# Performance work log

Measured on AMD Instinct MI355X. Metric: run time of the kernel, lower is better.

The kernel has to match this reference:

```python
import jax, jax.numpy as jnp
import numpy as np

N, E, B = 30000, 480000, 64
F_IN, HID, ED = 128, 64, 32
NEG, EPS = 0.2, 1e-5


def _add_self_loops(edge_index, edge_attr):
    # PyG add_self_loops with fill_value='mean': self-loop edge_attr of node i
    # is the mean of edge_attr over edges whose destination is i.
    src, dst = edge_index[0], edge_index[1]
    cnt = jax.ops.segment_sum(jnp.ones((edge_attr.shape[0],), edge_attr.dtype), dst, num_segments=N)
    mean = jax.ops.segment_sum(edge_attr, dst, num_segments=N) / jnp.maximum(cnt, 1.0)[:, None]
    loop = jnp.arange(N)
    return jnp.concatenate([src, loop]), jnp.concatenate([dst, loop]), jnp.concatenate([edge_attr, mean], axis=0)


def _gat_conv(x, src, dst, ea, W, We, a_s, a_d, a_e, bias, H, Fo):
    xs = (x @ W).reshape(-1, H, Fo)              # [N, H, Fo]
    al_src = (xs * a_s).sum(-1)                  # [N, H]
    al_dst = (xs * a_d).sum(-1)                  # [N, H]
    ef = (ea @ We).reshape(-1, H, Fo)            # [Et, H, Fo]
    alpha = al_src[src] + al_dst[dst] + (ef * a_e).sum(-1)   # [Et, H]
    alpha = jax.nn.leaky_relu(alpha, NEG)
    # softmax over incoming edges of each destination node (segment softmax)
    m = jax.ops.segment_max(alpha, dst, num_segments=N)
    ex = jnp.exp(alpha - m[dst])
    s = jax.ops.segment_sum(ex, dst, num_segments=N)
    w = ex / s[dst]                              # [Et, H]
    out = jax.ops.segment_sum(xs[src] * w[:, :, None], dst, num_segments=N)
    return out.reshape(-1, H * Fo) + bias


def _bn(x, g, b):
    # BatchNorm1d in training mode: biased batch statistics over nodes
    mu = x.mean(0)
    var = x.var(0)
    return (x - mu) * jax.lax.rsqrt(var + EPS) * g + b


def _pool(x, batch, Wg, bg):
    # GlobalAttention: softmax(gate_nn(x)) per graph, weighted sum of x
    gate = (x @ Wg + bg)[:, 0]                   # [N]
    m = jax.ops.segment_max(gate, batch, num_segments=B)
    e = jnp.exp(gate - m[batch])
    s = jax.ops.segment_sum(e, batch, num_segments=B)
    w = e / s[batch]
    return jax.ops.segment_sum(x * w[:, None], batch, num_segments=B)   # [B, HID]


def setup_inputs():
    k = jax.random.split(jax.random.key(0), 16)
    g = lambda i, shape, fan: jax.random.normal(k[i], shape, jnp.float32) / np.sqrt(fan)
    return {
        "x": jax.random.normal(k[0], (N, F_IN), jnp.float32),
        "edge_attr": jax.random.normal(k[1], (E, ED), jnp.float32),
        "edge_index": jax.random.randint(k[2], (2, E), 0, N),
        "batch": jnp.sort(jax.random.randint(k[3], (N,), 0, B)),
        "W1": g(4, (F_IN, 4 * HID), F_IN),
        "We1": g(5, (ED, 4 * HID), ED),
        "att_src1": g(6, (4, HID), HID),
        "att_dst1": g(7, (4, HID), HID),
        "att_edge1": g(8, (4, HID), HID),
        "bias1": jnp.zeros((4 * HID,), jnp.float32),
        "g1": jnp.ones((4 * HID,), jnp.float32),
        "b1": jnp.zeros((4 * HID,), jnp.float32),
        "W2": g(9, (4 * HID, HID), 4 * HID),
        "We2": g(10, (ED, HID), ED),
        "att_src2": g(11, (1, HID), HID),
        "att_dst2": g(12, (1, HID), HID),
        "att_edge2": g(13, (1, HID), HID),
        "bias2": jnp.zeros((HID,), jnp.float32),
        "g2": jnp.ones((HID,), jnp.float32),
        "b2": jnp.zeros((HID,), jnp.float32),
        "Wg": g(14, (HID, 1), HID),
        "bg": jnp.zeros((1,), jnp.float32),
    }


def reference(x, edge_attr, edge_index, batch, W1, We1, att_src1, att_dst1, att_edge1, bias1, g1, b1, W2, We2, att_src2, att_dst2, att_edge2, bias2, g2, b2, Wg, bg):
    src, dst, ea = _add_self_loops(edge_index, edge_attr)
    h = jax.nn.relu(_bn(_gat_conv(x, src, dst, ea, W1, We1, att_src1, att_dst1, att_edge1, bias1, 4, HID), g1, b1))
    h = jax.nn.relu(_bn(_gat_conv(h, src, dst, ea, W2, We2, att_src2, att_dst2, att_edge2, bias2, 1, HID), g2, b2))
    return _pool(h, batch, Wg, bg)
```

## Files before the change

kernel.cpp:

```cpp
#include <hip/hip_runtime.h>
#include <math.h>

#define NN 30000
#define EE 480000
#define BB 64

typedef __bf16 b16x8 __attribute__((ext_vector_type(8)));
typedef float  f32x4 __attribute__((ext_vector_type(4)));
typedef unsigned short u16x8 __attribute__((ext_vector_type(8)));

__device__ __forceinline__ float wsum64(float v){
  #pragma unroll
  for (int m = 32; m >= 1; m >>= 1) v += __shfl_xor(v, m, 64);
  return v;
}
__device__ __forceinline__ float wmax64(float v){
  #pragma unroll
  for (int m = 32; m >= 1; m >>= 1) v = fmaxf(v, __shfl_xor(v, m, 64));
  return v;
}
__device__ __forceinline__ float wsum16(float v){
  #pragma unroll
  for (int m = 1; m < 16; m <<= 1) v += __shfl_xor(v, m, 64);
  return v;
}
__device__ __forceinline__ unsigned short f2b(float f){
  union { float f; unsigned u; } v; v.f = f;
  unsigned r = v.u + 0x7fffu + ((v.u >> 16) & 1u);
  return (unsigned short)(r >> 16);
}
__device__ __forceinline__ float b2f(unsigned short u){
  union { unsigned u; float f; } v; v.u = ((unsigned)u) << 16;
  return v.f;
}

__global__ void hist_kernel(const int* __restrict__ dst, int* __restrict__ deg){
  int e = blockIdx.x*256 + threadIdx.x;
  if (e < EE) atomicAdd(&deg[dst[e]], 1);
}

__global__ __launch_bounds__(1024) void scan_kernel(const int* __restrict__ deg, int* __restrict__ rowptr){
  __shared__ int s[1024];
  int tid = threadIdx.x;
  const int PER = 30;
  int base = tid * PER;
  int sum = 0;
  for (int j = 0; j < PER; j++){ int idx = base+j; if (idx < NN) sum += deg[idx]; }
  s[tid] = sum; __syncthreads();
  for (int off = 1; off < 1024; off <<= 1){
    int v = 0;
    if (tid >= off) v = s[tid-off];
    __syncthreads();
    s[tid] += v;
    __syncthreads();
  }
  int run = s[tid] - sum;
  for (int j = 0; j < PER; j++){
    int idx = base+j;
    if (idx < NN){ rowptr[idx] = run; run += deg[idx]; }
  }
  if (tid == 1023) rowptr[NN] = s[1023];
}

__global__ void prep_kernel(const float* __restrict__ W1, const float* __restrict__ W2,
                            const float* __restrict__ We1, const float* __restrict__ ae1,
                            const float* __restrict__ We2, const float* __restrict__ ae2,
                            unsigned short* __restrict__ W1t, unsigned short* __restrict__ W2t,
                            float* __restrict__ wae){
  int t = threadIdx.x;
  if (blockIdx.x == 0){
    for (int k = 0; k < 128; k++) W1t[t*128 + k] = f2b(W1[k*256 + t]);
    if (t < 64){
      for (int k = 0; k < 256; k++) W2t[t*256 + k] = f2b(W2[k*64 + t]);
    }
  } else {
    if (t < 128){
      int h = t >> 5, k = t & 31;
      float s = 0.f;
      for (int f = 0; f < 64; f++) s += We1[k*256 + h*64 + f] * ae1[h*64 + f];
      wae[h*32 + k] = s;
    } else if (t < 160){
      int k = t - 128;
      float s = 0.f;
      for (int f = 0; f < 64; f++) s += We2[k*64 + f] * ae2[f];
      wae[128 + k] = s;
    }
  }
}

__global__ __launch_bounds__(256) void edot_scatter_kernel(const float* __restrict__ ea,
    const float* __restrict__ wae, const int* __restrict__ src, const int* __restrict__ dst,
    const int* __restrict__ rowptr, int* __restrict__ cursor,
    int* __restrict__ srccsr, float* __restrict__ edot1, float* __restrict__ edot2){
  __shared__ float s_w[160];
  if (threadIdx.x < 160) s_w[threadIdx.x] = wae[threadIdx.x];
  __syncthreads();
  const int il = threadIdx.x & 7;
  const int e = blockIdx.x*32 + (threadIdx.x >> 3);
  if (e >= EE) return;
  float4 v = *(const float4*)(ea + (size_t)e*32 + il*4);
  float dots[5];
  #pragma unroll
  for (int h = 0; h < 5; h++){
    float4 w = *(const float4*)&s_w[h*32 + il*4];
    dots[h] = v.x*w.x + v.y*w.y + v.z*w.z + v.w*w.w;
  }
  #pragma unroll
  for (int m = 1; m < 8; m <<= 1)
    #pragma unroll
    for (int h = 0; h < 5; h++) dots[h] += __shfl_xor(dots[h], m, 64);
  if (il == 0){
    int dd = dst[e];
    int slot = rowptr[dd] + atomicAdd(&cursor[dd], 1);
    srccsr[slot] = src[e];
    float4 o; o.x = dots[0]; o.y = dots[1]; o.z = dots[2]; o.w = dots[3];
    *(float4*)(edot1 + (size_t)slot*4) = o;
    edot2[slot] = dots[4];
  }
}

__global__ __launch_bounds__(256) void gemm1_mfma(const float* __restrict__ x,
    const unsigned short* __restrict__ Bt, const float* __restrict__ a_s, const float* __restrict__ a_d,
    unsigned short* __restrict__ out, float* __restrict__ alsrc, float* __restrict__ aldst){
  __shared__ unsigned short As[128*136];
  __shared__ unsigned short Bs[64*136];
  const int tid = threadIdx.x;
  const int w = tid >> 6, lane = tid & 63;
  const int c = lane & 15, gq = lane >> 4;
  const int m0 = blockIdx.x * 128;
  #pragma unroll
  for (int q = 0; q < 16; q++){
    int ch = tid*16 + q;
    int r = ch >> 5, off = (ch & 31)*4;
    int grow = m0 + r;
    ushort4 o;
    if (grow < NN){
      float4 v = *(const float4*)(x + (size_t)grow*128 + off);
      o.x = f2b(v.x); o.y = f2b(v.y); o.z = f2b(v.z); o.w = f2b(v.w);
    } else o = make_ushort4(0,0,0,0);
    *(ushort4*)&As[r*136 + off] = o;
  }
  #pragma unroll
  for (int q = 0; q < 4; q++){
    int ch = tid*4 + q;
    int n = ch >> 4, off = (ch & 15)*8;
    *(ulonglong2*)&Bs[n*136 + off] = *(const ulonglong2*)(Bt + (size_t)n*128 + off);
  }
  __syncthreads();
  for (int head = 0; head < 4; head++){
    f32x4 acc[2][4];
    #pragma unroll
    for (int mt = 0; mt < 2; mt++)
      #pragma unroll
      for (int nt = 0; nt < 4; nt++) acc[mt][nt] = (f32x4){0.f,0.f,0.f,0.f};
    #pragma unroll
    for (int k0 = 0; k0 < 128; k0 += 32){
      b16x8 afr[2], bfr[4];
      #pragma unroll
      for (int mt = 0; mt < 2; mt++)
        afr[mt] = *(const b16x8*)&As[(w*32 + mt*16 + c)*136 + k0 + gq*8];
      #pragma unroll
      for (int nt = 0; nt < 4; nt++)
        bfr[nt] = *(const b16x8*)&Bs[(nt*16 + c)*136 + k0 + gq*8];
      #pragma unroll
      for (int mt = 0; mt < 2; mt++)
        #pragma unroll
        for (int nt = 0; nt < 4; nt++)
          acc[mt][nt] = __builtin_amdgcn_mfma_f32_16x16x32_bf16(afr[mt], bfr[nt], acc[mt][nt], 0, 0, 0);
    }
    __syncthreads();
    if (head < 3){
      #pragma unroll
      for (int q = 0; q < 4; q++){
        int ch = tid*4 + q;
        int n = ch >> 4, off = (ch & 15)*8;
        *(ulonglong2*)&Bs[n*136 + off] = *(const ulonglong2*)(Bt + (size_t)((head+1)*64 + n)*128 + off);
      }
    }
    float asv[4], adv[4];
    #pragma unroll
    for (int nt = 0; nt < 4; nt++){
      asv[nt] = a_s[head*64 + nt*16 + c];
      adv[nt] = a_d[head*64 + nt*16 + c];
    }
    #pragma unroll
    for (int mt = 0; mt < 2; mt++){
      int base_row = m0 + w*32 + mt*16 + gq*4;
      #pragma unroll
      for (int r = 0; r < 4; r++){
        int row = base_row + r;
        float ps = 0.f, pd = 0.f;
        #pragma unroll
        for (int nt = 0; nt < 4; nt++){
          ps += acc[mt][nt][r] * asv[nt];
          pd += acc[mt][nt][r] * adv[nt];
        }
        ps = wsum16(ps); pd = wsum16(pd);
        if (row < NN){
          if (c == 0){
            alsrc[(size_t)row*4 + head] = ps;
            aldst[(size_t)row*4 + head] = pd;
          }
          #pragma unroll
          for (int nt = 0; nt < 4; nt++)
            out[(size_t)row*256 + head*64 + nt*16 + c] = f2b(acc[mt][nt][r]);
        }
      }
    }
    if (head < 3) __syncthreads();
  }
}

__global__ __launch_bounds__(256) void gemm2_mfma(const unsigned short* __restrict__ Ab,
    const unsigned short* __restrict__ Bt,
    const float* __restrict__ cs, const float* __restrict__ csq,
    const float* __restrict__ g, const float* __restrict__ b,
    const float* __restrict__ a_s, const float* __restrict__ a_d,
    unsigned short* __restrict__ out, float* __restrict__ alsrc, float* __restrict__ aldst){
  __shared__ unsigned short As[128*136];
  __shared__ unsigned short Bs[64*136];
  __shared__ float s_scale[256], s_shift[256];
  const int tid = threadIdx.x;
  const int w = tid >> 6, lane = tid & 63;
  const int c = lane & 15, gq = lane >> 4;
  const int m0 = blockIdx.x * 128;
  if (tid < 256){
    float mu  = cs[tid]  * (1.f/NN);
    float var = csq[tid] * (1.f/NN) - mu*mu;
    float rs  = rsqrtf(var + 1e-5f);
    float sc  = rs * g[tid];
    s_scale[tid] = sc;
    s_shift[tid] = b[tid] - mu*sc;
  }
  __syncthreads();
  f32x4 acc[2][4];
  #pragma unroll
  for (int mt = 0; mt < 2; mt++)
    #pragma unroll
    for (int nt = 0; nt < 4; nt++) acc[mt][nt] = (f32x4){0.f,0.f,0.f,0.f};
  for (int kp = 0; kp < 256; kp += 128){
    #pragma unroll
    for (int q = 0; q < 16; q++){
      int ch = tid*16 + q;
      int r = ch >> 5, off = (ch & 31)*4;
      int grow = m0 + r;
      ushort4 o;
      if (grow < NN){
        ushort4 v = *(const ushort4*)(Ab + (size_t)grow*256 + kp + off);
        float4 sc = *(const float4*)&s_scale[kp + off];
        float4 sh = *(const float4*)&s_shift[kp + off];
        o.x = f2b(fmaxf(fmaf(b2f(v.x), sc.x, sh.x), 0.f));
        o.y = f2b(fmaxf(fmaf(b2f(v.y), sc.y, sh.y), 0.f));
        o.z = f2b(fmaxf(fmaf(b2f(v.z), sc.z, sh.z), 0.f));
        o.w = f2b(fmaxf(fmaf(b2f(v.w), sc.w, sh.w), 0.f));
      } else o = make_ushort4(0,0,0,0);
      *(ushort4*)&As[r*136 + off] = o;
    }
    #pragma unroll
    for (int q = 0; q < 4; q++){
      int ch = tid*4 + q;
      int n = ch >> 4, off = (ch & 15)*8;
      *(ulonglong2*)&Bs[n*136 + off] = *(const ulonglong2*)(Bt + (size_t)n*256 + kp + off);
    }
    __syncthreads();
    #pragma unroll
    for (int k0 = 0; k0 < 128; k0 += 32){
      b16x8 afr[2], bfr[4];
      #pragma unroll
      for (int mt = 0; mt < 2; mt++)
        afr[mt] = *(const b16x8*)&As[(w*32 + mt*16 + c)*136 + k0 + gq*8];
      #pragma unroll
      for (int nt = 0; nt < 4; nt++)
        bfr[nt] = *(const b16x8*)&Bs[(nt*16 + c)*136 + k0 + gq*8];
      #pragma unroll
      for (int mt = 0; mt < 2; mt++)
        #pragma unroll
        for (int nt = 0; nt < 4; nt++)
          acc[mt][nt] = __builtin_amdgcn_mfma_f32_16x16x32_bf16(afr[mt], bfr[nt], acc[mt][nt], 0, 0, 0);
    }
    __syncthreads();
  }
  float asv[4], adv[4];
  #pragma unroll
  for (int nt = 0; nt < 4; nt++){
    asv[nt] = a_s[nt*16 + c];
    adv[nt] = a_d[nt*16 + c];
  }
  #pragma unroll
  for (int mt = 0; mt < 2; mt++){
    int base_row = m0 + w*32 + mt*16 + gq*4;
    #pragma unroll
    for (int r = 0; r < 4; r++){
      int row = base_row + r;
      float ps = 0.f, pd = 0.f;
      #pragma unroll
      for (int nt = 0; nt < 4; nt++){
        ps += acc[mt][nt][r] * asv[nt];
        pd += acc[mt][nt][r] * adv[nt];
      }
      ps = wsum16(ps); pd = wsum16(pd);
      if (row < NN){
        if (c == 0){
          alsrc[row] = ps;
          aldst[row] = pd;
        }
        #pragma unroll
        for (int nt = 0; nt < 4; nt++)
          out[(size_t)row*64 + nt*16 + c] = f2b(acc[mt][nt][r]);
      }
    }
  }
}

template<int H>
__global__ __launch_bounds__(256) void agg_kernel(const int* __restrict__ rowptr,
    const int* __restrict__ src_csr, const float* __restrict__ edot,
    const float* __restrict__ al_src, const float* __restrict__ al_dst,
    const unsigned short* __restrict__ xsb, const float* __restrict__ bias,
    unsigned short* __restrict__ outb, float* __restrict__ outf){
  constexpr int CH = 128;
  __shared__ float s_e_all[4][CH*H];
  __shared__ int   s_src_all[4][CH];
  const int wid  = threadIdx.x >> 6;
  const int lane = threadIdx.x & 63;
  const int i = blockIdx.x*4 + wid;
  float* s_e  = s_e_all[wid];
  int*   s_src = s_src_all[wid];
  const int r0 = rowptr[i];
  const int d  = rowptr[i+1] - r0;
  float ad[H], asi[H];
  #pragma unroll
  for (int h = 0; h < H; h++){ ad[h] = al_dst[(size_t)i*H+h]; asi[h] = al_src[(size_t)i*H+h]; }
  float sesum[H], m[H];
  #pragma unroll
  for (int h = 0; h < H; h++){ sesum[h] = 0.f; m[h] = -1e30f; }
  for (int t = lane; t < d; t += 64){
    int s = r0 + t;
    int sn = src_csr[s];
    if (t < CH) s_src[t] = sn;
    float al[H];
    if constexpr (H == 4){
      float4 av = *(const float4*)(al_src + (size_t)sn*4);
      float4 ev = *(const float4*)(edot + (size_t)s*4);
      al[0]=av.x+ad[0]+ev.x; al[1]=av.y+ad[1]+ev.y; al[2]=av.z+ad[2]+ev.z; al[3]=av.w+ad[3]+ev.w;
      sesum[0]+=ev.x; sesum[1]+=ev.y; sesum[2]+=ev.z; sesum[3]+=ev.w;
    } else {
      float ev = edot[s];
      al[0] = al_src[sn] + ad[0] + ev;
      sesum[0] += ev;
    }
    #pragma unroll
    for (int h = 0; h < H; h++){
      float a = al[h]; a = a > 0.f ? a : 0.2f*a;
      if (t < CH) s_e[t*H+h] = a;
      m[h] = fmaxf(m[h], a);
    }
  }
  float invd = (d > 0) ? 1.f/(float)d : 0.f;
  float sa[H];
  #pragma unroll
  for (int h = 0; h < H; h++){
    sesum[h] = wsum64(sesum[h]);
    m[h] = wmax64(m[h]);
    float a = asi[h] + ad[h] + sesum[h]*invd;
    sa[h] = a > 0.f ? a : 0.2f*a;
    m[h] = fmaxf(m[h], sa[h]);
  }
  float acc8[8];
  #pragma unroll
  for (int j = 0; j < 8; j++) acc8[j] = 0.f;
  float dpart[H];
  #pragma unroll
  for (int h = 0; h < H; h++) dpart[h] = 0.f;
  const int half = lane >> 5, il5 = lane & 31;
  const int grp  = lane >> 3, il3 = lane & 7;
  int c0 = 0;
  while (c0 < d){
    int cl = min(CH, d - c0);
    if (c0 > 0){
      for (int t = lane; t < cl; t += 64){
        int s = r0 + c0 + t;
        int sn = src_csr[s];
        s_src[t] = sn;
        if constexpr (H == 4){
          float4 av = *(const float4*)(al_src + (size_t)sn*4);
          float4 ev = *(const float4*)(edot + (size_t)s*4);
          float a0=av.x+ad[0]+ev.x, a1=av.y+ad[1]+ev.y, a2=av.z+ad[2]+ev.z, a3=av.w+ad[3]+ev.w;
          s_e[t*4+0]=a0>0.f?a0:0.2f*a0; s_e[t*4+1]=a1>0.f?a1:0.2f*a1;
          s_e[t*4+2]=a2>0.f?a2:0.2f*a2; s_e[t*4+3]=a3>0.f?a3:0.2f*a3;
        } else {
          float a = al_src[sn] + ad[0] + edot[s];
          s_e[t] = a > 0.f ? a : 0.2f*a;
        }
      }
    }
    for (int t = lane; t < cl; t += 64){
      #pragma unroll
      for (int h = 0; h < H; h++){
        float e = __expf(s_e[t*H+h] - m[h]);
        s_e[t*H+h] = e;
        dpart[h] += e;
      }
    }
    __builtin_amdgcn_wave_barrier();
    if constexpr (H == 4){
      const int hd = il5 >> 3;
      for (int t = half; t < cl; t += 2){
        int sn = s_src[t];
        float wv = s_e[t*4 + hd];
        u16x8 u = *(const u16x8*)(xsb + (size_t)sn*256 + il5*8);
        #pragma unroll
        for (int j = 0; j < 8; j++) acc8[j] += wv * b2f(u[j]);
      }
    } else {
      for (int t = grp; t < cl; t += 8){
        int sn = s_src[t];
        float wv = s_e[t];
        u16x8 u = *(const u16x8*)(xsb + (size_t)sn*64 + il3*8);
        #pragma unroll
        for (int j = 0; j < 8; j++) acc8[j] += wv * b2f(u[j]);
      }
    }
    __builtin_amdgcn_wave_barrier();
    c0 += CH;
  }
  float es[H];
  #pragma unroll
  for (int h = 0; h < H; h++) es[h] = __expf(sa[h] - m[h]);
  if (lane == 0){
    #pragma unroll
    for (int h = 0; h < H; h++) dpart[h] += es[h];
  }
  if constexpr (H == 4){
    if (half == 0){
      float wv = es[il5 >> 3];
      u16x8 u = *(const u16x8*)(xsb + (size_t)i*256 + il5*8);
      #pragma unroll
      for (int j = 0; j < 8; j++) acc8[j] += wv * b2f(u[j]);
    }
  } else {
    if (grp == 0){
      float wv = es[0];
      u16x8 u = *(const u16x8*)(xsb + (size_t)i*64 + il3*8);
      #pragma unroll
      for (int j = 0; j < 8; j++) acc8[j] += wv * b2f(u[j]);
    }
  }
  float denom[H];
  #pragma unroll
  for (int h = 0; h < H; h++) denom[h] = wsum64(dpart[h]);
  if constexpr (H == 4){
    #pragma unroll
    for (int j = 0; j < 8; j++) acc8[j] += __shfl_xor(acc8[j], 32, 64);
    if (lane < 32){
      float inv = 1.f / denom[il5 >> 3];
      u16x8 o;
      #pragma unroll
      for (int j = 0; j < 8; j++) o[j] = f2b(acc8[j]*inv + bias[il5*8 + j]);
      *(u16x8*)(outb + (size_t)i*256 + il5*8) = o;
    }
  } else {
    #pragma unroll
    for (int j = 0; j < 8; j++){
      acc8[j] += __shfl_xor(acc8[j], 8, 64);
      acc8[j] += __shfl_xor(acc8[j], 16, 64);
      acc8[j] += __shfl_xor(acc8[j], 32, 64);
    }
    if (lane < 8){
      float inv = 1.f / denom[0];
      float4 o0, o1;
      o0.x = acc8[0]*inv + bias[il3*8+0]; o0.y = acc8[1]*inv + bias[il3*8+1];
      o0.z = acc8[2]*inv + bias[il3*8+2]; o0.w = acc8[3]*inv + bias[il3*8+3];
      o1.x = acc8[4]*inv + bias[il3*8+4]; o1.y = acc8[5]*inv + bias[il3*8+5];
      o1.z = acc8[6]*inv + bias[il3*8+6]; o1.w = acc8[7]*inv + bias[il3*8+7];
      *(float4*)(outf + (size_t)i*64 + il3*8)     = o0;
      *(float4*)(outf + (size_t)i*64 + il3*8 + 4) = o1;
    }
  }
}

__global__ __launch_bounds__(256) void bn_stats_b16_kernel(const unsigned short* __restrict__ h,
    float* __restrict__ cs, float* __restrict__ csq){
  __shared__ float s_red[4][256], q_red[4][256];
  const int tid = threadIdx.x;
  const int wv = tid >> 6, lane = tid & 63;
  const int rg = lane >> 5, cg = lane & 31;
  float s8[8], q8[8];
  #pragma unroll
  for (int j = 0; j < 8; j++){ s8[j] = 0.f; q8[j] = 0.f; }
  for (int chunk = blockIdx.x; chunk < 3750; chunk += 256){
    int r = chunk*8 + wv*2 + rg;
    u16x8 u = *(const u16x8*)(h + (size_t)r*256 + cg*8);
    #pragma unroll
    for (int j = 0; j < 8; j++){
      float v = b2f(u[j]);
      s8[j] += v; q8[j] += v*v;
    }
  }
  #pragma unroll
  for (int j = 0; j < 8; j++){
    s8[j] += __shfl_xor(s8[j], 32, 64);
    q8[j] += __shfl_xor(q8[j], 32, 64);
  }
  if (lane < 32){
    #pragma unroll
    for (int j = 0; j < 8; j++){
      s_red[wv][cg*8 + j] = s8[j];
      q_red[wv][cg*8 + j] = q8[j];
    }
  }
  __syncthreads();
  if (tid < 256){
    float ts = s_red[0][tid] + s_red[1][tid] + s_red[2][tid] + s_red[3][tid];
    float tq = q_red[0][tid] + q_red[1][tid] + q_red[2][tid] + q_red[3][tid];
    atomicAdd(&cs[tid], ts);
    atomicAdd(&csq[tid], tq);
  }
}

__global__ __launch_bounds__(256) void bn_stats_f32_kernel(const float* __restrict__ h,
    float* __restrict__ cs, float* __restrict__ csq){
  int col = threadIdx.x & 63;
  int ro  = threadIdx.x >> 6;
  float s = 0.f, s2 = 0.f;
  for (int r = blockIdx.x*4 + ro; r < NN; r += 1024){
    float v = h[(size_t)r*64 + col];
    s += v; s2 += v*v;
  }
  atomicAdd(&cs[col], s);
  atomicAdd(&csq[col], s2);
}

__global__ __launch_bounds__(256) void gate_kernel(const float* __restrict__ h,
    const float* __restrict__ cs, const float* __restrict__ csq,
    const float* __restrict__ g2, const float* __restrict__ b2,
    const float* __restrict__ Wg, const float* __restrict__ bg,
    float* __restrict__ hn, float* __restrict__ gate){
  int wid = threadIdx.x >> 6, lane = threadIdx.x & 63;
  int n = blockIdx.x*4 + wid;
  float mu  = cs[lane]  * (1.f/NN);
  float var = csq[lane] * (1.f/NN) - mu*mu;
  float rs  = rsqrtf(var + 1e-5f);
  float sc  = rs * g2[lane];
  float sh  = b2[lane] - mu*sc;
  float v = h[(size_t)n*64 + lane];
  float xx = fmaxf(fmaf(v, sc, sh), 0.f);
  hn[(size_t)n*64 + lane] = xx;
  float p = wsum64(xx * Wg[lane]);
  if (lane == 0) gate[n] = p + bg[0];
}

__global__ __launch_bounds__(256) void pool_kernel(const int* __restrict__ batch,
    const float* __restrict__ gate, const float* __restrict__ hn, float* __restrict__ out){
  __shared__ float red[256];
  __shared__ float a_red[4][64], w_red[4];
  __shared__ int seb[2];
  int b = blockIdx.x, tid = threadIdx.x;
  int wv = tid >> 6, lane = tid & 63;
  if (tid < 2){
    int target = b + tid;
    int lo = 0, hi = NN;
    while (lo < hi){ int mid = (lo+hi) >> 1; if (batch[mid] < target) lo = mid+1; else hi = mid; }
    seb[tid] = lo;
  }
  __syncthreads();
  int s = seb[0], e = seb[1];
  if (e <= s){ if (tid < 64) out[b*64 + tid] = 0.f; return; }
  float mloc = -1e30f;
  for (int n = s + tid; n < e; n += 256) mloc = fmaxf(mloc, gate[n]);
  mloc = wmax64(mloc);
  if (lane == 0) red[wv] = mloc;
  __syncthreads();
  float m = fmaxf(fmaxf(red[0], red[1]), fmaxf(red[2], red[3]));
  int rgrp = tid >> 4, cq = tid & 15;
  f32x4 acc = (f32x4){0.f,0.f,0.f,0.f};
  float wp = 0.f;
  for (int n = s + rgrp; n < e; n += 16){
    float wgt = __expf(gate[n] - m);
    float4 v = *(const float4*)(hn + (size_t)n*64 + cq*4);
    acc[0] += wgt*v.x; acc[1] += wgt*v.y; acc[2] += wgt*v.z; acc[3] += wgt*v.w;
    if (cq == 0) wp += wgt;
  }
  #pragma unroll
  for (int j = 0; j < 4; j++){
    acc[j] += __shfl_xor(acc[j], 16, 64);
    acc[j] += __shfl_xor(acc[j], 32, 64);
  }
  wp += __shfl_xor(wp, 16, 64);
  wp += __shfl_xor(wp, 32, 64);
  if (lane < 16){
    #pragma unroll
    for (int j = 0; j < 4; j++) a_red[wv][lane*4 + j] = acc[j];
  }
  if (lane == 0) w_red[wv] = wp;
  __syncthreads();
  if (tid < 64){
    float tot = a_red[0][tid] + a_red[1][tid] + a_red[2][tid] + a_red[3][tid];
    float wsm = w_red[0] + w_red[1] + w_red[2] + w_red[3];
    out[b*64 + tid] = tot / wsm;
  }
}

extern "C" void kernel_launch(void* const* d_in, const int* in_sizes, int n_in,
                              void* d_out, int out_size, void* d_ws, size_t ws_size,
                              hipStream_t stream){
  const float* x     = (const float*)d_in[0];
  const float* ea    = (const float*)d_in[1];
  const int*   ei    = (const int*)d_in[2];
  const int*   batch = (const int*)d_in[3];
  const float* W1    = (const float*)d_in[4];
  const float* We1   = (const float*)d_in[5];
  const float* as1   = (const float*)d_in[6];
  const float* ad1   = (const float*)d_in[7];
  const float* ae1   = (const float*)d_in[8];
  const float* bias1 = (const float*)d_in[9];
  const float* g1    = (const float*)d_in[10];
  const float* b1    = (const float*)d_in[11];
  const float* W2    = (const float*)d_in[12];
  const float* We2   = (const float*)d_in[13];
  const float* as2   = (const float*)d_in[14];
  const float* ad2   = (const float*)d_in[15];
  const float* ae2   = (const float*)d_in[16];
  const float* bias2 = (const float*)d_in[17];
  const float* g2    = (const float*)d_in[18];
  const float* b2    = (const float*)d_in[19];
  const float* Wg    = (const float*)d_in[20];
  const float* bg    = (const float*)d_in[21];
  const int* srcI = ei;
  const int* dstI = ei + EE;

  char* ws = (char*)d_ws;
  int*   deg    = (int*)(ws + 0);
  int*   cursor = (int*)(ws + 120064);
  float* stats  = (float*)(ws + 240128);
  int*   rowptr = (int*)(ws + 244224);
  int*   srccsr = (int*)(ws + 364288);
  float* wae    = (float*)(ws + 2284288);
  unsigned short* W1t = (unsigned short*)(ws + 2285056);
  unsigned short* W2t = (unsigned short*)(ws + 2350592);
  float* alsrc  = (float*)(ws + 2383360);
  float* aldst  = (float*)(ws + 2863360);
  float* gateb  = (float*)(ws + 3343360);
  float* edot1  = (float*)(ws + 3463424);
  float* edot2  = (float*)(ws + 11143424);
  unsigned short* xs1b = (unsigned short*)(ws + 13063424);
  unsigned short* h1b  = (unsigned short*)(ws + 28423424);
  unsigned short* xs2b = (unsigned short*)(ws + 43783424);
  float* h2     = (float*)(ws + 47623424);
  float* hn     = (float*)(ws + 55303424);

  (void)hipMemsetAsync(ws, 0, 244224, stream);

  hist_kernel<<<1875, 256, 0, stream>>>(dstI, deg);
  scan_kernel<<<1, 1024, 0, stream>>>(deg, rowptr);
  prep_kernel<<<2, 256, 0, stream>>>(W1, W2, We1, ae1, We2, ae2, W1t, W2t, wae);
  edot_scatter_kernel<<<15000, 256, 0, stream>>>(ea, wae, srcI, dstI, rowptr, cursor,
                                                 srccsr, edot1, edot2);

  gemm1_mfma<<<235, 256, 0, stream>>>(x, W1t, as1, ad1, xs1b, alsrc, aldst);
  agg_kernel<4><<<7500, 256, 0, stream>>>(rowptr, srccsr, edot1, alsrc, aldst, xs1b, bias1, h1b, nullptr);
  bn_stats_b16_kernel<<<256, 256, 0, stream>>>(h1b, stats + 0, stats + 256);

  gemm2_mfma<<<235, 256, 0, stream>>>(h1b, W2t, stats + 0, stats + 256, g1, b1,
                                      as2, ad2, xs2b, alsrc, aldst);
  agg_kernel<1><<<7500, 256, 0, stream>>>(rowptr, srccsr, edot2, alsrc, aldst, xs2b, bias2, nullptr, h2);
  bn_stats_f32_kernel<<<256, 256, 0, stream>>>(h2, stats + 512, stats + 576);

  gate_kernel<<<7500, 256, 0, stream>>>(h2, stats + 512, stats + 576, g2, b2, Wg, bg, hn, gateb);
  pool_kernel<<<64, 256, 0, stream>>>(batch, gateb, hn, (float*)d_out);
}
```

Before: 420.7 us.

## Parallelize scan and weight prep, pack CSR edge records into 32-byte structs

The single-block degree scan becomes a 118-block scan in which each block recomputes its prefix offset by summing all earlier degrees. The weight transpose in prep_kernel is spread across 385 blocks instead of 2 serial-loop blocks. The CSR source index and both edge-dot arrays are packed into one 8-float record per edge, so the scatter does fewer scattered writes and the aggregation kernels read a single line per edge. The trade-off is redundant prefix reads in the scan and a padded record that carries unused bytes.

```diff
diff --git a/kernel.cpp b/kernel.cpp
--- a/kernel.cpp
+++ b/kernel.cpp
@@ -39,27 +39,30 @@
   if (e < EE) atomicAdd(&deg[dst[e]], 1);
 }
 
-__global__ __launch_bounds__(1024) void scan_kernel(const int* __restrict__ deg, int* __restrict__ rowptr){
-  __shared__ int s[1024];
-  int tid = threadIdx.x;
-  const int PER = 30;
-  int base = tid * PER;
-  int sum = 0;
-  for (int j = 0; j < PER; j++){ int idx = base+j; if (idx < NN) sum += deg[idx]; }
-  s[tid] = sum; __syncthreads();
-  for (int off = 1; off < 1024; off <<= 1){
-    int v = 0;
-    if (tid >= off) v = s[tid-off];
+__global__ __launch_bounds__(256) void scan_kernel(const int* __restrict__ deg, int* __restrict__ rowptr){
+  __shared__ int s[256];
+  __shared__ int wred[4];
+  const int b = blockIdx.x, tid = threadIdx.x;
+  const int base = b*256;
+  int part = 0;
+  for (int idx = tid; idx < base; idx += 256) part += deg[idx];
+  #pragma unroll
+  for (int m = 32; m >= 1; m >>= 1) part += __shfl_xor(part, m, 64);
+  if ((tid & 63) == 0) wred[tid >> 6] = part;
+  __syncthreads();
+  int offset = wred[0] + wred[1] + wred[2] + wred[3];
+  int n = base + tid;
+  int d = (n < NN) ? deg[n] : 0;
+  s[tid] = d;
+  __syncthreads();
+  for (int off = 1; off < 256; off <<= 1){
+    int v = (tid >= off) ? s[tid - off] : 0;
     __syncthreads();
     s[tid] += v;
     __syncthreads();
   }
-  int run = s[tid] - sum;
-  for (int j = 0; j < PER; j++){
-    int idx = base+j;
-    if (idx < NN){ rowptr[idx] = run; run += deg[idx]; }
-  }
-  if (tid == 1023) rowptr[NN] = s[1023];
+  if (n < NN) rowptr[n] = offset + s[tid] - d;
+  if (b == 0 && tid == 0) rowptr[NN] = EE;
 }
 
 __global__ void prep_kernel(const float* __restrict__ W1, const float* __restrict__ W2,
@@ -67,12 +70,12 @@
                             const float* __restrict__ We2, const float* __restrict__ ae2,
                             unsigned short* __restrict__ W1t, unsigned short* __restrict__ W2t,
                             float* __restrict__ wae){
-  int t = threadIdx.x;
-  if (blockIdx.x == 0){
-    for (int k = 0; k < 128; k++) W1t[t*128 + k] = f2b(W1[k*256 + t]);
-    if (t < 64){
-      for (int k = 0; k < 256; k++) W2t[t*256 + k] = f2b(W2[k*64 + t]);
-    }
+  int t = threadIdx.x, b = blockIdx.x;
+  if (b < 128){
+    W1t[t*128 + b] = f2b(W1[b*256 + t]);
+  } else if (b < 384){
+    int k = b - 128;
+    if (t < 64) W2t[t*256 + k] = f2b(W2[k*64 + t]);
   } else {
     if (t < 128){
       int h = t >> 5, k = t & 31;
@@ -90,12 +93,12 @@
 
 __global__ __launch_bounds__(256) void edot_scatter_kernel(const float* __restrict__ ea,
     const float* __restrict__ wae, const int* __restrict__ src, const int* __restrict__ dst,
-    const int* __restrict__ rowptr, int* __restrict__ cursor,
-    int* __restrict__ srccsr, float* __restrict__ edot1, float* __restrict__ edot2){
+    const int* __restrict__ rowptr, int* __restrict__ cursor, float* __restrict__ rec){
   __shared__ float s_w[160];
   if (threadIdx.x < 160) s_w[threadIdx.x] = wae[threadIdx.x];
   __syncthreads();
-  const int il = threadIdx.x & 7;
+  const int lane = threadIdx.x & 63;
+  const int il = lane & 7;
   const int e = blockIdx.x*32 + (threadIdx.x >> 3);
   if (e >= EE) return;
   float4 v = *(const float4*)(ea + (size_t)e*32 + il*4);
@@ -109,13 +112,18 @@
   for (int m = 1; m < 8; m <<= 1)
     #pragma unroll
     for (int h = 0; h < 5; h++) dots[h] += __shfl_xor(dots[h], m, 64);
+  int slot = 0;
   if (il == 0){
     int dd = dst[e];
-    int slot = rowptr[dd] + atomicAdd(&cursor[dd], 1);
-    srccsr[slot] = src[e];
-    float4 o; o.x = dots[0]; o.y = dots[1]; o.z = dots[2]; o.w = dots[3];
-    *(float4*)(edot1 + (size_t)slot*4) = o;
-    edot2[slot] = dots[4];
+    slot = rowptr[dd] + atomicAdd(&cursor[dd], 1);
+  }
+  slot = __shfl(slot, lane & ~7, 64);
+  if (il == 0){
+    float4 lo; lo.x = dots[0]; lo.y = dots[1]; lo.z = dots[2]; lo.w = dots[3];
+    *(float4*)(rec + (size_t)slot*8) = lo;
+  } else if (il == 1){
+    float4 hi; hi.x = dots[4]; hi.y = __int_as_float(src[e]); hi.z = 0.f; hi.w = 0.f;
+    *(float4*)(rec + (size_t)slot*8 + 4) = hi;
   }
 }
 
@@ -314,7 +322,7 @@
 
 template<int H>
 __global__ __launch_bounds__(256) void agg_kernel(const int* __restrict__ rowptr,
-    const int* __restrict__ src_csr, const float* __restrict__ edot,
+    const float* __restrict__ rec,
     const float* __restrict__ al_src, const float* __restrict__ al_dst,
     const unsigned short* __restrict__ xsb, const float* __restrict__ bias,
     unsigned short* __restrict__ outb, float* __restrict__ outf){
@@ -335,20 +343,23 @@
   #pragma unroll
   for (int h = 0; h < H; h++){ sesum[h] = 0.f; m[h] = -1e30f; }
   for (int t = lane; t < d; t += 64){
-    int s = r0 + t;
-    int sn = src_csr[s];
-    if (t < CH) s_src[t] = sn;
+    const float* rp = rec + (size_t)(r0 + t)*8;
     float al[H];
+    int sn;
     if constexpr (H == 4){
+      float4 ev = *(const float4*)rp;
+      float2 hi = *(const float2*)(rp + 4);
+      sn = __float_as_int(hi.y);
       float4 av = *(const float4*)(al_src + (size_t)sn*4);
-      float4 ev = *(const float4*)(edot + (size_t)s*4);
       al[0]=av.x+ad[0]+ev.x; al[1]=av.y+ad[1]+ev.y; al[2]=av.z+ad[2]+ev.z; al[3]=av.w+ad[3]+ev.w;
       sesum[0]+=ev.x; sesum[1]+=ev.y; sesum[2]+=ev.z; sesum[3]+=ev.w;
     } else {
-      float ev = edot[s];
-      al[0] = al_src[sn] + ad[0] + ev;
-      sesum[0] += ev;
-    }
+      float2 hi = *(const float2*)(rp + 4);
+      sn = __float_as_int(hi.y);
+      al[0] = al_src[sn] + ad[0] + hi.x;
+      sesum[0] += hi.x;
+    }
+    if (t < CH) s_src[t] = sn;
     #pragma unroll
     for (int h = 0; h < H; h++){
       float a = al[h]; a = a > 0.f ? a : 0.2f*a;
@@ -379,17 +390,21 @@
     int cl = min(CH, d - c0);
     if (c0 > 0){
       for (int t = lane; t < cl; t += 64){
-        int s = r0 + c0 + t;
-        int sn = src_csr[s];
-        s_src[t] = sn;
+        const float* rp = rec + (size_t)(r0 + c0 + t)*8;
         if constexpr (H == 4){
+          float4 ev = *(const float4*)rp;
+          float2 hi = *(const float2*)(rp + 4);
+          int sn = __float_as_int(hi.y);
+          s_src[t] = sn;
           float4 av = *(const float4*)(al_src + (size_t)sn*4);
-          float4 ev = *(const float4*)(edot + (size_t)s*4);
           float a0=av.x+ad[0]+ev.x, a1=av.y+ad[1]+ev.y, a2=av.z+ad[2]+ev.z, a3=av.w+ad[3]+ev.w;
           s_e[t*4+0]=a0>0.f?a0:0.2f*a0; s_e[t*4+1]=a1>0.f?a1:0.2f*a1;
           s_e[t*4+2]=a2>0.f?a2:0.2f*a2; s_e[t*4+3]=a3>0.f?a3:0.2f*a3;
         } else {
-          float a = al_src[sn] + ad[0] + edot[s];
+          float2 hi = *(const float2*)(rp + 4);
+          int sn = __float_as_int(hi.y);
+          s_src[t] = sn;
+          float a = al_src[sn] + ad[0] + hi.x;
           s_e[t] = a > 0.f ? a : 0.2f*a;
         }
       }
@@ -634,36 +649,33 @@
   int*   cursor = (int*)(ws + 120064);
   float* stats  = (float*)(ws + 240128);
   int*   rowptr = (int*)(ws + 244224);
-  int*   srccsr = (int*)(ws + 364288);
-  float* wae    = (float*)(ws + 2284288);
-  unsigned short* W1t = (unsigned short*)(ws + 2285056);
-  unsigned short* W2t = (unsigned short*)(ws + 2350592);
-  float* alsrc  = (float*)(ws + 2383360);
-  float* aldst  = (float*)(ws + 2863360);
-  float* gateb  = (float*)(ws + 3343360);
-  float* edot1  = (float*)(ws + 3463424);
-  float* edot2  = (float*)(ws + 11143424);
-  unsigned short* xs1b = (unsigned short*)(ws + 13063424);
-  unsigned short* h1b  = (unsigned short*)(ws + 28423424);
-  unsigned short* xs2b = (unsigned short*)(ws + 43783424);
-  float* h2     = (float*)(ws + 47623424);
-  float* hn     = (float*)(ws + 55303424);
+  float* wae    = (float*)(ws + 364288);
+  unsigned short* W1t = (unsigned short*)(ws + 365056);
+  unsigned short* W2t = (unsigned short*)(ws + 430592);
+  float* alsrc  = (float*)(ws + 463360);
+  float* aldst  = (float*)(ws + 943360);
+  float* gateb  = (float*)(ws + 1423360);
+  float* rec    = (float*)(ws + 1543424);
+  unsigned short* xs1b = (unsigned short*)(ws + 16903424);
+  unsigned short* h1b  = (unsigned short*)(ws + 32263424);
+  unsigned short* xs2b = (unsigned short*)(ws + 47623424);
+  float* h2     = (float*)(ws + 51463424);
+  float* hn     = (float*)(ws + 59143424);
 
   (void)hipMemsetAsync(ws, 0, 244224, stream);
 
   hist_kernel<<<1875, 256, 0, stream>>>(dstI, deg);
-  scan_kernel<<<1, 1024, 0, stream>>>(deg, rowptr);
-  prep_kernel<<<2, 256, 0, stream>>>(W1, W2, We1, ae1, We2, ae2, W1t, W2t, wae);
-  edot_scatter_kernel<<<15000, 256, 0, stream>>>(ea, wae, srcI, dstI, rowptr, cursor,
-                                                 srccsr, edot1, edot2);
+  scan_kernel<<<118, 256, 0, stream>>>(deg, rowptr);
+  prep_kernel<<<385, 256, 0, stream>>>(W1, W2, We1, ae1, We2, ae2, W1t, W2t, wae);
+  edot_scatter_kernel<<<15000, 256, 0, stream>>>(ea, wae, srcI, dstI, rowptr, cursor, rec);
 
   gemm1_mfma<<<235, 256, 0, stream>>>(x, W1t, as1, ad1, xs1b, alsrc, aldst);
-  agg_kernel<4><<<7500, 256, 0, stream>>>(rowptr, srccsr, edot1, alsrc, aldst, xs1b, bias1, h1b, nullptr);
+  agg_kernel<4><<<7500, 256, 0, stream>>>(rowptr, rec, alsrc, aldst, xs1b, bias1, h1b, nullptr);
   bn_stats_b16_kernel<<<256, 256, 0, stream>>>(h1b, stats + 0, stats + 256);
 
   gemm2_mfma<<<235, 256, 0, stream>>>(h1b, W2t, stats + 0, stats + 256, g1, b1,
                                       as2, ad2, xs2b, alsrc, aldst);
-  agg_kernel<1><<<7500, 256, 0, stream>>>(rowptr, srccsr, edot2, alsrc, aldst, xs2b, bias2, nullptr, h2);
+  agg_kernel<1><<<7500, 256, 0, stream>>>(rowptr, rec, alsrc, aldst, xs2b, bias2, nullptr, h2);
   bn_stats_f32_kernel<<<256, 256, 0, stream>>>(h2, stats + 512, stats + 576);
 
   gate_kernel<<<7500, 256, 0, stream>>>(h2, stats + 512, stats + 576, g2, b2, Wg, bg, hn, gateb);
```

After: 364.4 us. 1.15x faster.
